# Optimization experiments

Hardware: AMD Instinct MI355X
Metric: run time of the kernel (lower is better)

## Reference

```python
import jax, jax.numpy as jnp
import numpy as np
from jax import lax
from jax.scipy.special import logsumexp

B, T, S = 256, 1024, 64


def setup_inputs() -> dict:
    key = jax.random.key(0)
    k1, k2, k3, k4 = jax.random.split(key, 4)
    return {
        "observations": jax.random.randint(k1, (B, T), 0, S, dtype=jnp.int64 if jax.config.jax_enable_x64 else jnp.int32),
        "log_transition_matrix": jax.random.normal(k2, (S, S), dtype=jnp.float32),
        "log_initial_probs": jax.random.normal(k3, (S,), dtype=jnp.float32),
        "log_emission_probs": jax.random.normal(k4, (S,), dtype=jnp.float32),
    }


def reference(observations, log_transition_matrix, log_initial_probs, log_emission_probs):
    # per-(batch, time) scalar emission log-prob, (B, T)
    emis = log_emission_probs[observations]

    # ---- forward recurrence (alpha) ----
    alpha0 = log_initial_probs[None, :] + emis[:, 0][:, None]  # (B, S)

    def fstep(a_prev, e_t):
        # a_prev: (B, S); logsumexp over previous state axis
        a_new = logsumexp(a_prev[:, :, None] + log_transition_matrix[None, :, :], axis=1) + e_t[:, None]
        return a_new, a_new

    _, alphas = lax.scan(fstep, alpha0, emis[:, 1:].T)  # alphas: (T-1, B, S)
    alpha = jnp.concatenate([alpha0[:, None, :], jnp.moveaxis(alphas, 0, 1)], axis=1)  # (B, T, S)

    # ---- backward recurrence (beta) ----
    beta_last = jnp.zeros((B, S), dtype=alpha.dtype)

    def bstep(b_next, e_t1):
        # logsumexp over next state axis (axis=2)
        b_new = logsumexp(b_next[:, None, :] + log_transition_matrix[None, :, :] + e_t1[:, None, None], axis=2)
        return b_new, b_new

    # xs[t] = emis[:, t+1] for t = 0..T-2; reverse scan so carry flows T-1 -> 0
    _, betas = lax.scan(bstep, beta_last, emis[:, 1:].T, reverse=True)  # (T-1, B, S), betas[t] = beta_t
    beta = jnp.concatenate([jnp.moveaxis(betas, 0, 1), beta_last[:, None, :]], axis=1)  # (B, T, S)

    log_gamma = alpha + beta
    return jax.nn.log_softmax(log_gamma, axis=2)
```

## Files before the change

kernel.cpp:

```cpp
#include <hip/hip_runtime.h>


#define TT 1024
#define NK 10

__device__ __forceinline__ void fma4(float4& acc, float a, float4 b) {
    acc.x = fmaf(a, b.x, acc.x);
    acc.y = fmaf(a, b.y, acc.y);
    acc.z = fmaf(a, b.z, acc.z);
    acc.w = fmaf(a, b.w, acc.w);
}

__global__ __launch_bounds__(256) void hmm_powers(const float* __restrict__ logA,
                                                  float* __restrict__ M,
                                                  float* __restrict__ Mt) {
    const int LD = 68;
    __shared__ float bufA[64 * 68];
    __shared__ float bufB[64 * 68];
    __shared__ float red4[4];
    const int tid  = threadIdx.x;
    const int wid  = tid >> 6;
    const int lane = tid & 63;

    float4 ev[4];
    float lmax = 0.f;
    #pragma unroll
    for (int c = 0; c < 4; ++c) {
        float4 v = ((const float4*)logA)[tid + 256 * c];
        float4 w;
        w.x = __expf(v.x); w.y = __expf(v.y); w.z = __expf(v.z); w.w = __expf(v.w);
        ev[c] = w;
        lmax = fmaxf(lmax, fmaxf(fmaxf(w.x, w.y), fmaxf(w.z, w.w)));
    }
    #pragma unroll
    for (int off = 32; off > 0; off >>= 1)
        lmax = fmaxf(lmax, __shfl_xor(lmax, off, 64));
    if (lane == 0) red4[wid] = lmax;
    __syncthreads();
    const float scale0 = 1.f / fmaxf(fmaxf(red4[0], red4[1]), fmaxf(red4[2], red4[3]));
    #pragma unroll
    for (int c = 0; c < 4; ++c) {
        int f = tid + 256 * c;
        int idx = f * 4;
        int i = idx >> 6;
        int j = idx & 63;
        float4 w = ev[c];
        w.x *= scale0; w.y *= scale0; w.z *= scale0; w.w *= scale0;
        *(float4*)&bufA[i * LD + j] = w;
        ((float4*)M)[f] = w;
        Mt[(j + 0) * 64 + i] = w.x;
        Mt[(j + 1) * 64 + i] = w.y;
        Mt[(j + 2) * 64 + i] = w.z;
        Mt[(j + 3) * 64 + i] = w.w;
    }

    float* cur = bufA;
    float* nxt = bufB;
    const int r0 = (tid >> 4) * 4, j0 = (tid & 15) * 4;

    for (int k = 1; k < NK; ++k) {
        __syncthreads();
        float4 acc0 = make_float4(0.f, 0.f, 0.f, 0.f);
        float4 acc1 = acc0, acc2 = acc0, acc3 = acc0;
        #pragma unroll
        for (int i0 = 0; i0 < 64; i0 += 4) {
            float4 a0 = *(const float4*)&cur[(r0 + 0) * LD + i0];
            float4 a1 = *(const float4*)&cur[(r0 + 1) * LD + i0];
            float4 a2 = *(const float4*)&cur[(r0 + 2) * LD + i0];
            float4 a3 = *(const float4*)&cur[(r0 + 3) * LD + i0];
            float4 b0 = *(const float4*)&cur[(i0 + 0) * LD + j0];
            float4 b1 = *(const float4*)&cur[(i0 + 1) * LD + j0];
            float4 b2 = *(const float4*)&cur[(i0 + 2) * LD + j0];
            float4 b3 = *(const float4*)&cur[(i0 + 3) * LD + j0];
            fma4(acc0, a0.x, b0); fma4(acc0, a0.y, b1); fma4(acc0, a0.z, b2); fma4(acc0, a0.w, b3);
            fma4(acc1, a1.x, b0); fma4(acc1, a1.y, b1); fma4(acc1, a1.z, b2); fma4(acc1, a1.w, b3);
            fma4(acc2, a2.x, b0); fma4(acc2, a2.y, b1); fma4(acc2, a2.z, b2); fma4(acc2, a2.w, b3);
            fma4(acc3, a3.x, b0); fma4(acc3, a3.y, b1); fma4(acc3, a3.z, b2); fma4(acc3, a3.w, b3);
        }
        float m0 = fmaxf(fmaxf(acc0.x, acc0.y), fmaxf(acc0.z, acc0.w));
        float m1 = fmaxf(fmaxf(acc1.x, acc1.y), fmaxf(acc1.z, acc1.w));
        float m2 = fmaxf(fmaxf(acc2.x, acc2.y), fmaxf(acc2.z, acc2.w));
        float m3 = fmaxf(fmaxf(acc3.x, acc3.y), fmaxf(acc3.z, acc3.w));
        float m = fmaxf(fmaxf(m0, m1), fmaxf(m2, m3));
        #pragma unroll
        for (int off = 32; off > 0; off >>= 1)
            m = fmaxf(m, __shfl_xor(m, off, 64));
        if (lane == 0) red4[wid] = m;
        __syncthreads();
        const float sc = 1.f / fmaxf(fmaxf(red4[0], red4[1]), fmaxf(red4[2], red4[3]));
        float* Mk  = M  + (k << 12);
        float* Mtk = Mt + (k << 12);
        float4 accs[4] = {acc0, acc1, acc2, acc3};
        #pragma unroll
        for (int rr = 0; rr < 4; ++rr) {
            float4 w = accs[rr];
            w.x *= sc; w.y *= sc; w.z *= sc; w.w *= sc;
            *(float4*)&nxt[(r0 + rr) * LD + j0] = w;
            *(float4*)&Mk[(r0 + rr) * 64 + j0] = w;
            Mtk[(j0 + 0) * 64 + r0 + rr] = w.x;
            Mtk[(j0 + 1) * 64 + r0 + rr] = w.y;
            Mtk[(j0 + 2) * 64 + r0 + rr] = w.z;
            Mtk[(j0 + 3) * 64 + r0 + rr] = w.w;
        }
        float* tmp = cur; cur = nxt; nxt = tmp;
    }
}

__global__ __launch_bounds__(128) void hmm_rows(const float* __restrict__ M,
                                                const float* __restrict__ Mt,
                                                const float* __restrict__ logInit,
                                                float* __restrict__ SG) {
    const int t = blockIdx.x;
    __shared__ float sp[64];
    __shared__ float sq[64];
    const int lane = threadIdx.x & 63;
    const int w    = threadIdx.x >> 6;

    if (w == 0) {
        sp[lane] = __expf(logInit[lane]);
        const int e = t;
        for (int k = 0; k < NK; ++k) {
            if ((e >> k) & 1) {
                const float* Mk = M + (k << 12);
                float a0 = 0.f, a1 = 0.f, a2 = 0.f, a3 = 0.f;
                #pragma unroll
                for (int i = 0; i < 16; ++i) {
                    a0 = fmaf(sp[i],      Mk[( i       << 6) + lane], a0);
                    a1 = fmaf(sp[i + 16], Mk[((i + 16) << 6) + lane], a1);
                    a2 = fmaf(sp[i + 32], Mk[((i + 32) << 6) + lane], a2);
                    a3 = fmaf(sp[i + 48], Mk[((i + 48) << 6) + lane], a3);
                }
                float acc = (a0 + a1) + (a2 + a3);
                float mx = acc;
                #pragma unroll
                for (int off = 32; off > 0; off >>= 1)
                    mx = fmaxf(mx, __shfl_xor(mx, off, 64));
                sp[lane] = acc * (1.f / mx);
            }
        }
    } else {
        sq[lane] = 1.f;
        const int e = (TT - 1) - t;
        for (int k = 0; k < NK; ++k) {
            if ((e >> k) & 1) {
                const float* Mk = Mt + (k << 12);
                float a0 = 0.f, a1 = 0.f, a2 = 0.f, a3 = 0.f;
                #pragma unroll
                for (int i = 0; i < 16; ++i) {
                    a0 = fmaf(sq[i],      Mk[( i       << 6) + lane], a0);
                    a1 = fmaf(sq[i + 16], Mk[((i + 16) << 6) + lane], a1);
                    a2 = fmaf(sq[i + 32], Mk[((i + 32) << 6) + lane], a2);
                    a3 = fmaf(sq[i + 48], Mk[((i + 48) << 6) + lane], a3);
                }
                float acc = (a0 + a1) + (a2 + a3);
                float mx = acc;
                #pragma unroll
                for (int off = 32; off > 0; off >>= 1)
                    mx = fmaxf(mx, __shfl_xor(mx, off, 64));
                sq[lane] = acc * (1.f / mx);
            }
        }
    }
    __syncthreads();

    if (w == 0) {
        float gv = __logf(sp[lane]) + __logf(sq[lane]);
        float mx = gv;
        #pragma unroll
        for (int off = 32; off > 0; off >>= 1)
            mx = fmaxf(mx, __shfl_xor(mx, off, 64));
        float ex = __expf(gv - mx);
        float sm = ex;
        #pragma unroll
        for (int off = 32; off > 0; off >>= 1)
            sm += __shfl_xor(sm, off, 64);
        SG[(t << 6) + lane] = gv - mx - __logf(sm);
    }
}

__global__ __launch_bounds__(256) void hmm_bcast(const float* __restrict__ SG,
                                                 float* __restrict__ out) {
    const int c  = blockIdx.x;
    const int b  = c >> 3;
    const int tc = c & 7;
    const float4* s4 = (const float4*)SG + ((size_t)tc << 11);
    float4*       o4 = (float4*)out + ((size_t)b << 14) + ((size_t)tc << 11);
    const int tid = threadIdx.x;
    #pragma unroll
    for (int it = 0; it < 8; ++it) {
        int f = tid + (it << 8);
        o4[f] = s4[f];
    }
}

extern "C" void kernel_launch(void* const* d_in, const int* in_sizes, int n_in,
                              void* d_out, int out_size, void* d_ws, size_t ws_size,
                              hipStream_t stream) {
    const float* logA    = (const float*)d_in[1];
    const float* logInit = (const float*)d_in[2];
    float* M  = (float*)d_ws;
    float* Mt = M + NK * 4096;
    float* SG = Mt + NK * 4096;
    hmm_powers<<<1, 256, 0, stream>>>(logA, M, Mt);
    hmm_rows<<<TT, 128, 0, stream>>>(M, Mt, logInit, SG);
    hmm_bcast<<<2048, 256, 0, stream>>>(SG, (float*)d_out);
}
```

Measured before the change: 121.5 us.

## Compute matrix powers with split-bf16 MFMA instead of scalar FP32 FMA

Each squaring step in hmm_powers now runs as matrix-core work (mfma_f32_16x16x32_bf16) rather than scalar FP32 FMA. To keep near-FP32 accuracy, each value is split into a bf16 high part and a bf16 low part, and three MFMA products are summed. Row-major and transposed bf16 copies are kept in padded LDS so both operands load as contiguous 8-element vectors. The aim is to shorten the serial single-block power chain, at the cost of extra conversion work, scalar LDS scatter stores, and a small loss of precision from dropping the lo*lo term.

Result: faster. 109.8 us (-9.6%).

```diff
diff --git a/kernel.cpp b/kernel.cpp
--- a/kernel.cpp
+++ b/kernel.cpp
@@ -3,85 +3,89 @@
 
 #define TT 1024
 #define NK 10
-
-__device__ __forceinline__ void fma4(float4& acc, float a, float4 b) {
-    acc.x = fmaf(a, b.x, acc.x);
-    acc.y = fmaf(a, b.y, acc.y);
-    acc.z = fmaf(a, b.z, acc.z);
-    acc.w = fmaf(a, b.w, acc.w);
+#define PS 72
+
+typedef short  bf16x8 __attribute__((ext_vector_type(8)));
+typedef float  f32x4  __attribute__((ext_vector_type(4)));
+
+__device__ __forceinline__ unsigned short f2bf(float x) {
+    unsigned u = __float_as_uint(x);
+    unsigned r = u + 0x7fffu + ((u >> 16) & 1u);
+    return (unsigned short)(r >> 16);
+}
+__device__ __forceinline__ float bf2f(unsigned short h) {
+    return __uint_as_float(((unsigned)h) << 16);
 }
 
 __global__ __launch_bounds__(256) void hmm_powers(const float* __restrict__ logA,
                                                   float* __restrict__ M,
                                                   float* __restrict__ Mt) {
-    const int LD = 68;
-    __shared__ float bufA[64 * 68];
-    __shared__ float bufB[64 * 68];
+    __shared__ unsigned short Ah[64 * PS], Al[64 * PS];
+    __shared__ unsigned short Th[64 * PS], Tl[64 * PS];
     __shared__ float red4[4];
     const int tid  = threadIdx.x;
     const int wid  = tid >> 6;
     const int lane = tid & 63;
 
-    float4 ev[4];
-    float lmax = 0.f;
-    #pragma unroll
-    for (int c = 0; c < 4; ++c) {
-        float4 v = ((const float4*)logA)[tid + 256 * c];
-        float4 w;
-        w.x = __expf(v.x); w.y = __expf(v.y); w.z = __expf(v.z); w.w = __expf(v.w);
-        ev[c] = w;
-        lmax = fmaxf(lmax, fmaxf(fmaxf(w.x, w.y), fmaxf(w.z, w.w)));
-    }
-    #pragma unroll
-    for (int off = 32; off > 0; off >>= 1)
-        lmax = fmaxf(lmax, __shfl_xor(lmax, off, 64));
-    if (lane == 0) red4[wid] = lmax;
-    __syncthreads();
-    const float scale0 = 1.f / fmaxf(fmaxf(red4[0], red4[1]), fmaxf(red4[2], red4[3]));
-    #pragma unroll
-    for (int c = 0; c < 4; ++c) {
-        int f = tid + 256 * c;
-        int idx = f * 4;
-        int i = idx >> 6;
-        int j = idx & 63;
-        float4 w = ev[c];
-        w.x *= scale0; w.y *= scale0; w.z *= scale0; w.w *= scale0;
-        *(float4*)&bufA[i * LD + j] = w;
-        ((float4*)M)[f] = w;
-        Mt[(j + 0) * 64 + i] = w.x;
-        Mt[(j + 1) * 64 + i] = w.y;
-        Mt[(j + 2) * 64 + i] = w.z;
-        Mt[(j + 3) * 64 + i] = w.w;
-    }
-
-    float* cur = bufA;
-    float* nxt = bufB;
-    const int r0 = (tid >> 4) * 4, j0 = (tid & 15) * 4;
+    {
+        const int row = tid >> 2;
+        const int c0  = (tid & 3) * 16;
+        float v[16];
+        float lmax = 0.f;
+        #pragma unroll
+        for (int jj = 0; jj < 4; ++jj) {
+            float4 x = ((const float4*)logA)[row * 16 + (tid & 3) * 4 + jj];
+            float e0 = __expf(x.x), e1 = __expf(x.y), e2 = __expf(x.z), e3 = __expf(x.w);
+            v[4 * jj + 0] = e0; v[4 * jj + 1] = e1; v[4 * jj + 2] = e2; v[4 * jj + 3] = e3;
+            lmax = fmaxf(lmax, fmaxf(fmaxf(e0, e1), fmaxf(e2, e3)));
+        }
+        #pragma unroll
+        for (int off = 32; off > 0; off >>= 1)
+            lmax = fmaxf(lmax, __shfl_xor(lmax, off, 64));
+        if (lane == 0) red4[wid] = lmax;
+        __syncthreads();
+        const float sc = 1.f / fmaxf(fmaxf(red4[0], red4[1]), fmaxf(red4[2], red4[3]));
+        #pragma unroll
+        for (int j = 0; j < 16; ++j) {
+            float val = v[j] * sc;
+            unsigned short hi = f2bf(val);
+            unsigned short lo = f2bf(val - bf2f(hi));
+            int cc = c0 + j;
+            Ah[row * PS + cc] = hi;  Al[row * PS + cc] = lo;
+            Th[cc * PS + row] = hi;  Tl[cc * PS + row] = lo;
+            M [row * 64 + cc] = val;
+            Mt[cc * 64 + row] = val;
+        }
+    }
+
+    const int quad = (lane >> 4);
+    const int l15  = lane & 15;
 
     for (int k = 1; k < NK; ++k) {
         __syncthreads();
-        float4 acc0 = make_float4(0.f, 0.f, 0.f, 0.f);
-        float4 acc1 = acc0, acc2 = acc0, acc3 = acc0;
-        #pragma unroll
-        for (int i0 = 0; i0 < 64; i0 += 4) {
-            float4 a0 = *(const float4*)&cur[(r0 + 0) * LD + i0];
-            float4 a1 = *(const float4*)&cur[(r0 + 1) * LD + i0];
-            float4 a2 = *(const float4*)&cur[(r0 + 2) * LD + i0];
-            float4 a3 = *(const float4*)&cur[(r0 + 3) * LD + i0];
-            float4 b0 = *(const float4*)&cur[(i0 + 0) * LD + j0];
-            float4 b1 = *(const float4*)&cur[(i0 + 1) * LD + j0];
-            float4 b2 = *(const float4*)&cur[(i0 + 2) * LD + j0];
-            float4 b3 = *(const float4*)&cur[(i0 + 3) * LD + j0];
-            fma4(acc0, a0.x, b0); fma4(acc0, a0.y, b1); fma4(acc0, a0.z, b2); fma4(acc0, a0.w, b3);
-            fma4(acc1, a1.x, b0); fma4(acc1, a1.y, b1); fma4(acc1, a1.z, b2); fma4(acc1, a1.w, b3);
-            fma4(acc2, a2.x, b0); fma4(acc2, a2.y, b1); fma4(acc2, a2.z, b2); fma4(acc2, a2.w, b3);
-            fma4(acc3, a3.x, b0); fma4(acc3, a3.y, b1); fma4(acc3, a3.z, b2); fma4(acc3, a3.w, b3);
-        }
-        float m0 = fmaxf(fmaxf(acc0.x, acc0.y), fmaxf(acc0.z, acc0.w));
-        float m1 = fmaxf(fmaxf(acc1.x, acc1.y), fmaxf(acc1.z, acc1.w));
-        float m2 = fmaxf(fmaxf(acc2.x, acc2.y), fmaxf(acc2.z, acc2.w));
-        float m3 = fmaxf(fmaxf(acc3.x, acc3.y), fmaxf(acc3.z, acc3.w));
-        float m = fmaxf(fmaxf(m0, m1), fmaxf(m2, m3));
+        f32x4 acc[4];
+        #pragma unroll
+        for (int c = 0; c < 4; ++c) acc[c] = (f32x4){0.f, 0.f, 0.f, 0.f};
+        #pragma unroll
+        for (int kk = 0; kk < 2; ++kk) {
+            const int ao = (16 * wid + l15) * PS + 32 * kk + quad * 8;
+            bf16x8 ah = *(const bf16x8*)&Ah[ao];
+            bf16x8 al = *(const bf16x8*)&Al[ao];
+            #pragma unroll
+            for (int c = 0; c < 4; ++c) {
+                const int bo = (16 * c + l15) * PS + 32 * kk + quad * 8;
+                bf16x8 bh = *(const bf16x8*)&Th[bo];
+                bf16x8 bl = *(const bf16x8*)&Tl[bo];
+                acc[c] = __builtin_amdgcn_mfma_f32_16x16x32_bf16(ah, bh, acc[c], 0, 0, 0);
+                acc[c] = __builtin_amdgcn_mfma_f32_16x16x32_bf16(ah, bl, acc[c], 0, 0, 0);
+                acc[c] = __builtin_amdgcn_mfma_f32_16x16x32_bf16(al, bh, acc[c], 0, 0, 0);
+            }
+        }
+        float m = 0.f;
+        #pragma unroll
+        for (int c = 0; c < 4; ++c)
+            #pragma unroll
+            for (int r = 0; r < 4; ++r) m = fmaxf(m, acc[c][r]);
         #pragma unroll
         for (int off = 32; off > 0; off >>= 1)
             m = fmaxf(m, __shfl_xor(m, off, 64));
@@ -90,19 +94,23 @@
         const float sc = 1.f / fmaxf(fmaxf(red4[0], red4[1]), fmaxf(red4[2], red4[3]));
         float* Mk  = M  + (k << 12);
         float* Mtk = Mt + (k << 12);
-        float4 accs[4] = {acc0, acc1, acc2, acc3};
-        #pragma unroll
-        for (int rr = 0; rr < 4; ++rr) {
-            float4 w = accs[rr];
-            w.x *= sc; w.y *= sc; w.z *= sc; w.w *= sc;
-            *(float4*)&nxt[(r0 + rr) * LD + j0] = w;
-            *(float4*)&Mk[(r0 + rr) * 64 + j0] = w;
-            Mtk[(j0 + 0) * 64 + r0 + rr] = w.x;
-            Mtk[(j0 + 1) * 64 + r0 + rr] = w.y;
-            Mtk[(j0 + 2) * 64 + r0 + rr] = w.z;
-            Mtk[(j0 + 3) * 64 + r0 + rr] = w.w;
-        }
-        float* tmp = cur; cur = nxt; nxt = tmp;
+        #pragma unroll
+        for (int c = 0; c < 4; ++c) {
+            #pragma unroll
+            for (int r = 0; r < 4; ++r) {
+                float val = acc[c][r] * sc;
+                const int rr = 16 * wid + quad * 4 + r;
+                const int cc = 16 * c   + l15;
+                Mk [rr * 64 + cc] = val;
+                Mtk[cc * 64 + rr] = val;
+                if (k < NK - 1) {
+                    unsigned short hi = f2bf(val);
+                    unsigned short lo = f2bf(val - bf2f(hi));
+                    Ah[rr * PS + cc] = hi;  Al[rr * PS + cc] = lo;
+                    Th[cc * PS + rr] = hi;  Tl[cc * PS + rr] = lo;
+                }
+            }
+        }
     }
 }
 
```
